# Kernel tuning notes

Measured on AMD Instinct MI355X. Metric: run time of the kernel, lower is better.

## Reference

```python
import jax, jax.numpy as jnp
import numpy as np

BANDWIDTH = 512.0


def _pairwise_lse(A, B, bandwidth):
    """logsumexp over all pairs of exp(-||a-b||^2 / bandwidth).

    Matches torch: vmap over rows b of B computing logsumexp over A,
    then logsumexp over those row results == single logsumexp over the
    full [Na, Nb] matrix of -sq_dist/bandwidth.
    """
    # squared distances via ||a||^2 + ||b||^2 - 2 a.b  (GEMM-dominated)
    a2 = jnp.sum(A * A, axis=-1)  # [Na]
    b2 = jnp.sum(B * B, axis=-1)  # [Nb]
    d2 = a2[:, None] + b2[None, :] - 2.0 * (A @ B.T)  # [Na, Nb]
    return jax.nn.logsumexp(-d2 / bandwidth)


def setup_inputs() -> dict:
    key = jax.random.key(0)
    kx, ky = jax.random.split(key)
    X = jax.random.normal(kx, (8192, 512), dtype=jnp.float32)
    Y = jax.random.normal(ky, (8192, 512), dtype=jnp.float32)
    return {"X": X, "Y": Y}


def reference(X, Y):
    n = X.shape[0]
    m = Y.shape[0]
    xx = (jnp.exp(_pairwise_lse(X, X, BANDWIDTH)) - n) / (n * (n - 1))
    xy = jnp.exp(_pairwise_lse(X, Y, BANDWIDTH)) / (n * m)
    yy = (jnp.exp(_pairwise_lse(Y, Y, BANDWIDTH)) - m) / (m * (m - 1))
    return xx - 2.0 * xy + yy
```

## Files before the change

### kernel.cpp

```cpp
#include <hip/hip_runtime.h>
#include <math.h>


#define D      512
#define BTM    128
#define BTN    256
#define BTNP   128
#define BK     16
#define KSTEPS (D / BK)

#define AHI 0
#define ALO 256
#define BHI 512
#define BLO 1024

typedef _Float16 half8 __attribute__((ext_vector_type(8)));
typedef __attribute__((ext_vector_type(8)))  short  short8;
typedef __attribute__((ext_vector_type(16))) float  f32x16;

union U4H8 { uint4 u; half8 h; };
union U4S8 { uint4 u; short8 s; };

__device__ __forceinline__ unsigned short bf16_rne(float x) {
    unsigned u = __float_as_uint(x);
    return (unsigned short)((u + 0x7fffu + ((u >> 16) & 1u)) >> 16);
}
__device__ __forceinline__ float bf16_f32(unsigned short b) {
    return __uint_as_float(((unsigned)b) << 16);
}
__device__ __forceinline__ void split8(const float v[8], uint4& hi, uint4& lo) {
    unsigned h[8], l[8];
    #pragma unroll
    for (int j = 0; j < 8; j++) {
        unsigned short bh = bf16_rne(v[j]);
        float r = v[j] - bf16_f32(bh);
        unsigned short bl = bf16_rne(r);
        h[j] = bh; l[j] = bl;
    }
    hi.x = h[0] | (h[1] << 16); hi.y = h[2] | (h[3] << 16);
    hi.z = h[4] | (h[5] << 16); hi.w = h[6] | (h[7] << 16);
    lo.x = l[0] | (l[1] << 16); lo.y = l[2] | (l[3] << 16);
    lo.z = l[4] | (l[5] << 16); lo.w = l[6] | (l[7] << 16);
}

__device__ __forceinline__ void lds16(const uint4* g, uint4* l) {
    __builtin_amdgcn_global_load_lds(
        (const __attribute__((address_space(1))) void*)g,
        (__attribute__((address_space(3))) void*)(unsigned int)(uintptr_t)(void*)l,
        16, 0, 0);
}

__global__ void init_kernel(double* accum, unsigned* minkey) {
    if (threadIdx.x < 3) accum[threadIdx.x] = 0.0;
    if (threadIdx.x < 4) minkey[threadIdx.x] = 0xFFFFFFFFu;
}

__global__ __launch_bounds__(256)
void convert_h_kernel(const float* __restrict__ X, const float* __restrict__ Y,
                      uint4* __restrict__ Xh, uint4* __restrict__ Yh, int npts) {
    const float* src = blockIdx.z ? Y : X;
    uint4*       dst = blockIdx.z ? Yh : Xh;
    const int ks = blockIdx.y;
    const int p  = blockIdx.x * 256 + threadIdx.x;
    if (p >= npts) return;
    const float* s = src + (size_t)p * D + ks * BK;
    float v[16];
    *(float4*)&v[0]  = *(const float4*)(s);
    *(float4*)&v[4]  = *(const float4*)(s + 4);
    *(float4*)&v[8]  = *(const float4*)(s + 8);
    *(float4*)&v[12] = *(const float4*)(s + 12);
    U4H8 a, b;
    #pragma unroll
    for (int j = 0; j < 8; j++) { a.h[j] = (_Float16)v[j]; b.h[j] = (_Float16)v[8 + j]; }
    size_t u = (size_t)ks * npts * 2 + (size_t)(p >> 5) * 64 + (p & 31);
    dst[u] = a.u; dst[u + 32] = b.u;
}

__global__ __launch_bounds__(256)
void row_norms_kernel(const float* __restrict__ X, const float* __restrict__ Y,
                      float* __restrict__ X2, float* __restrict__ Y2, int N, int M) {
    const int wave = threadIdx.x >> 6;
    const int lane = threadIdx.x & 63;
    const int row  = blockIdx.x * 4 + wave;
    const float* src; float* dst; int r;
    if (row < N)          { src = X; dst = X2; r = row; }
    else if (row < N + M) { src = Y; dst = Y2; r = row - N; }
    else return;
    const float* p = src + (size_t)r * D;
    float s = 0.f;
    #pragma unroll
    for (int c = 0; c < D; c += 64) {
        float v = p[c + lane];
        s = fmaf(v, v, s);
    }
    #pragma unroll
    for (int off = 32; off > 0; off >>= 1) s += __shfl_down(s, off);
    if (lane == 0) dst[r] = s;
}

__device__ inline unsigned float_key(float f) {
    unsigned u = __float_as_uint(f);
    return (u & 0x80000000u) ? ~u : (u | 0x80000000u);
}
__device__ inline float key_float(unsigned k) {
    return __uint_as_float((k & 0x80000000u) ? (k ^ 0x80000000u) : ~k);
}

__global__ __launch_bounds__(256)
void diag_min_bits_kernel(const float* __restrict__ X, const float* __restrict__ Y,
                          const float* __restrict__ X2, const float* __restrict__ Y2,
                          unsigned* __restrict__ minkey, int ngx) {
    int b = blockIdx.x;
    const float *src, *n2; int zidx;
    if (b < ngx) { src = X; n2 = X2; zidx = 0; }
    else         { src = Y; n2 = Y2; zidx = 2; b -= ngx; }

    const int tid  = threadIdx.x;
    const int wave = tid >> 6, lane = tid & 63;
    const int grp  = b * 4 + wave;
    const int fp   = lane & 31, fh = lane >> 5;
    const int pt   = grp * 32 + fp;
    const float* s = src + (size_t)pt * D + fh * 8;

    f32x16 acc;
    #pragma unroll
    for (int i = 0; i < 16; i++) acc[i] = 0.f;

    for (int ks = 0; ks < KSTEPS; ks++) {
        float v[8];
        *(float4*)&v[0] = *(const float4*)(s + ks * BK);
        *(float4*)&v[4] = *(const float4*)(s + ks * BK + 4);
        U4S8 hi, lo;
        split8(v, hi.u, lo.u);
        short8 ah = hi.s, al = lo.s;
        acc = __builtin_amdgcn_mfma_f32_32x32x16_bf16(ah, ah, acc, 0, 0, 0);
        acc = __builtin_amdgcn_mfma_f32_32x32x16_bf16(ah, al, acc, 0, 0, 0);
        acc = __builtin_amdgcn_mfma_f32_32x32x16_bf16(al, ah, acc, 0, 0, 0);
    }

    float dmin = 1e30f;
    if (fh == ((fp >> 2) & 1)) {
        int r = (fp & 3) + 4 * (fp >> 3);
        float av = acc[r];
        float rn = n2[pt];
        float cn = rn;
        float d2 = rn + cn - 2.0f * av;
        dmin = d2;
    }
    #pragma unroll
    for (int off = 32; off > 0; off >>= 1) dmin = fminf(dmin, __shfl_down(dmin, off));
    __shared__ float wm[4];
    __shared__ int   wz[4];
    if (lane == 0) { wm[wave] = dmin; wz[wave] = zidx; }
    __syncthreads();
    if (tid == 0)
        atomicMin(&minkey[wz[0]],
                  float_key(fminf(fminf(wm[0], wm[1]), fminf(wm[2], wm[3]))));
}

__global__ __launch_bounds__(256, 4)
void pair_exp_sum_kernel(const uint4* __restrict__ Xh, const uint4* __restrict__ Yh,
                         const float* __restrict__ X2, const float* __restrict__ Y2,
                         double* __restrict__ accum, float* __restrict__ bmin,
                         int N, int M) {
    const int z = blockIdx.z;
    const uint4 *Ah, *Bh; const float *An, *Bn; bool sym; int na, nb;
    if (z == 0)      { Ah = Xh; Bh = Xh; An = X2; Bn = X2; sym = true;  na = N; nb = N; }
    else if (z == 1) { Ah = Xh; Bh = Yh; An = X2; Bn = Y2; sym = false; na = N; nb = M; }
    else             { Ah = Yh; Bh = Yh; An = Y2; Bn = Y2; sym = true;  na = M; nb = M; }
    const int bi = blockIdx.x, bj = blockIdx.y;
    if (sym && bj < bi) return;

    __shared__ uint4  smem[2][1024];
    __shared__ float  smN[BTM + BTNP];
    __shared__ double wsum[4];
    __shared__ float  wmin[4];

    const int tid  = threadIdx.x;
    const int wave = tid >> 6, lane = tid & 63;
    const int wy = wave >> 1, wx = wave & 1;
    const int row0 = bi * BTM, col0 = bj * BTNP;

    if (tid < BTM) smN[tid] = An[row0 + tid];
    else           smN[tid] = Bn[col0 + tid - BTM];

    const size_t strideA = (size_t)na * 2;
    const size_t strideB = (size_t)nb * 2;
    const int sj = wave >> 1, skind = wave & 1;
    const uint4* gS = (skind ? Bh + (size_t)(col0 >> 5) * 64
                             : Ah + (size_t)(row0 >> 5) * 64) + lane;
    const size_t strideS = skind ? strideB : strideA;

    f32x16 acc[2][2];
    #pragma unroll
    for (int g = 0; g < 2; g++)
        #pragma unroll
        for (int c = 0; c < 2; c++)
            #pragma unroll
            for (int i = 0; i < 16; i++) acc[g][c][i] = 0.f;

    auto stage2 = [&](int buf, int ks) {
        const uint4* g = gS + (size_t)(ks + sj) * strideS;
        uint4* d = &smem[buf][sj * 512 + skind * 256 + lane];
        #pragma unroll
        for (int t = 0; t < 4; t++)
            lds16(g + t * 64, d + t * 64);
    };
    auto computeK = [&](const uint4* base) {
        const half8* p = (const half8*)base;
        half8 ah[2], bh[2];
        #pragma unroll
        for (int g = 0; g < 2; g++) ah[g] = p[(2 * wy + g) * 64 + lane];
        #pragma unroll
        for (int c = 0; c < 2; c++) bh[c] = p[256 + (2 * wx + c) * 64 + lane];
        #pragma unroll
        for (int g = 0; g < 2; g++)
            #pragma unroll
            for (int c = 0; c < 2; c++)
                acc[g][c] = __builtin_amdgcn_mfma_f32_32x32x16_f16(ah[g], bh[c], acc[g][c], 0, 0, 0);
    };

    stage2(0, 0);

    #pragma unroll
    for (int it = 1; it < KSTEPS / 2; it++) {
        stage2(it & 1, 2 * it);
        asm volatile("s_waitcnt vmcnt(4)" ::: "memory");
        __builtin_amdgcn_s_barrier();
        __builtin_amdgcn_sched_barrier(0);
        const int pb = (it - 1) & 1;
        computeK(&smem[pb][0]);
        computeK(&smem[pb][512]);
        asm volatile("s_waitcnt lgkmcnt(0)" ::: "memory");
        __builtin_amdgcn_s_barrier();
    }
    asm volatile("s_waitcnt vmcnt(0)" ::: "memory");
    __builtin_amdgcn_s_barrier();
    __builtin_amdgcn_sched_barrier(0);
    computeK(&smem[1][0]);
    computeK(&smem[1][512]);

    const float wgt = (sym && bj > bi) ? 2.f : 1.f;

    const int fp = lane & 31, fh = lane >> 5;
    double s = 0.0;
    float dmin = 1e30f;
    {
        const float* rowN = &smN[64 * wy];
        const float* colN = &smN[BTM + 64 * wx];
        const float kC = -0.0028177637517362567f;
        #pragma unroll
        for (int g = 0; g < 2; g++)
            #pragma unroll
            for (int c = 0; c < 2; c++) {
                float cn = colN[32 * c + fp];
                float rs = 0.f;
                #pragma unroll
                for (int r = 0; r < 16; r++) {
                    int r32 = (r & 3) + 8 * (r >> 2) + 4 * fh;
                    float d2 = rowN[32 * g + r32] + cn - 2.0f * acc[g][c][r];
                    dmin = fminf(dmin, d2);
                    rs += exp2f(d2 * kC);
                }
                s += (double)rs;
            }
        s *= (double)wgt;
    }

    #pragma unroll
    for (int off = 32; off > 0; off >>= 1) {
        s += __shfl_down(s, off);
        dmin = fminf(dmin, __shfl_down(dmin, off));
    }
    if (lane == 0) { wsum[wave] = s; wmin[wave] = dmin; }
    __syncthreads();
    if (tid == 0) {
        atomicAdd(&accum[z], wsum[0] + wsum[1] + wsum[2] + wsum[3]);
        if (z == 1)
            bmin[bi * gridDim.y + bj] = fminf(fminf(wmin[0], wmin[1]),
                                              fminf(wmin[2], wmin[3]));
    }
}

__global__ __launch_bounds__(256)
void xy_gmin_kernel(const float* __restrict__ bmin, float* __restrict__ gmin, int nblk) {
    float m = 1e30f;
    for (int i = threadIdx.x; i < nblk; i += 256) m = fminf(m, bmin[i]);
    #pragma unroll
    for (int off = 32; off > 0; off >>= 1) m = fminf(m, __shfl_down(m, off));
    __shared__ float wm[4];
    if ((threadIdx.x & 63) == 0) wm[threadIdx.x >> 6] = m;
    __syncthreads();
    if (threadIdx.x == 0) gmin[0] = fminf(fminf(wm[0], wm[1]), fminf(wm[2], wm[3]));
}

__global__ __launch_bounds__(1024)
void refine_min_kernel(const float* __restrict__ A, const float* __restrict__ B,
                       const float* __restrict__ An, const float* __restrict__ Bn,
                       const float* __restrict__ bmin, const float* __restrict__ gmin,
                       unsigned* __restrict__ minkey, int zidx, int nbj) {
    const int bi = blockIdx.x;
    const int bj = blockIdx.y;
    float bm = fminf(bmin[bi * nbj + 2 * bj], bmin[bi * nbj + 2 * bj + 1]);
    if (!(bm < gmin[0] + 0.5f)) return;
    const int row0 = bi * BTM, col0 = bj * BTN;

    __shared__ uint4 smem[1536];
    __shared__ float smN[BTM + BTN];
    __shared__ float wmin[16];

    const int tid  = threadIdx.x;
    const int wave = tid >> 6, lane = tid & 63;
    const int gy = wave & 3, cg0 = 2 * (wave >> 2);
    if (tid < BTM) smN[tid] = An[row0 + tid];
    if (tid < BTN) smN[BTM + tid] = Bn[col0 + tid];

    const int fp = lane & 31, fh = lane >> 5;
    const int au = (32 * gy + fp) * 2 + fh;
    int bu[2];
    #pragma unroll
    for (int c = 0; c < 2; c++) bu[c] = (32 * (cg0 + c) + fp) * 2 + fh;

    f32x16 acc[2];
    #pragma unroll
    for (int c = 0; c < 2; c++)
        #pragma unroll
        for (int i = 0; i < 16; i++) acc[c][i] = 0.f;

    for (int ks = 0; ks < KSTEPS; ks++) {
        __syncthreads();
        if (tid < 256) {
            const float* s = A + (size_t)(row0 + (tid >> 1)) * D + ks * BK + (tid & 1) * 8;
            float v[8];
            *(float4*)&v[0] = *(const float4*)s;
            *(float4*)&v[4] = *(const float4*)(s + 4);
            uint4 hi, lo; split8(v, hi, lo);
            smem[AHI + tid] = hi; smem[ALO + tid] = lo;
        } else if (tid < 768) {
            int u = tid - 256;
            const float* s = B + (size_t)(col0 + (u >> 1)) * D + ks * BK + (u & 1) * 8;
            float v[8];
            *(float4*)&v[0] = *(const float4*)s;
            *(float4*)&v[4] = *(const float4*)(s + 4);
            uint4 hi, lo; split8(v, hi, lo);
            smem[BHI + u] = hi; smem[BLO + u] = lo;
        }
        __syncthreads();
        {
            const short8* p = (const short8*)&smem[0];
            short8 ah = p[AHI + au], al = p[ALO + au];
            short8 bh[2], bl[2];
            #pragma unroll
            for (int c = 0; c < 2; c++) { bh[c] = p[BHI + bu[c]]; bl[c] = p[BLO + bu[c]]; }
            #pragma unroll
            for (int c = 0; c < 2; c++)
                acc[c] = __builtin_amdgcn_mfma_f32_32x32x16_bf16(ah, bh[c], acc[c], 0, 0, 0);
            #pragma unroll
            for (int c = 0; c < 2; c++)
                acc[c] = __builtin_amdgcn_mfma_f32_32x32x16_bf16(ah, bl[c], acc[c], 0, 0, 0);
            #pragma unroll
            for (int c = 0; c < 2; c++)
                acc[c] = __builtin_amdgcn_mfma_f32_32x32x16_bf16(al, bh[c], acc[c], 0, 0, 0);
        }
    }

    float dmin = 1e30f;
    const float* rowN = &smN[32 * gy];
    #pragma unroll
    for (int c = 0; c < 2; c++) {
        float cn = smN[BTM + 32 * (cg0 + c) + fp];
        #pragma unroll
        for (int r = 0; r < 16; r++) {
            int r32 = (r & 3) + 8 * (r >> 2) + 4 * fh;
            float d2 = rowN[r32] + cn - 2.0f * acc[c][r];
            dmin = fminf(dmin, d2);
        }
    }

    #pragma unroll
    for (int off = 32; off > 0; off >>= 1) dmin = fminf(dmin, __shfl_down(dmin, off));
    if (lane == 0) wmin[wave] = dmin;
    __syncthreads();
    if (tid == 0) {
        float m = wmin[0];
        #pragma unroll
        for (int w = 1; w < 16; w++) m = fminf(m, wmin[w]);
        atomicMin(&minkey[zidx], float_key(m));
    }
}

__global__ void finalize_kernel(const double* __restrict__ accum,
                                const unsigned* __restrict__ minkey,
                                float* __restrict__ out, int N, int M) {
    if (threadIdx.x == 0 && blockIdx.x == 0) {
        float Sp[3];
        #pragma unroll
        for (int z = 0; z < 3; z++) {
            float m = key_float(minkey[z]) * (-1.0f / 512.0f);
            double Sshift = accum[z] * exp(-(double)m);
            float r = (float)log(Sshift);
            float lse = r + m;
            Sp[z] = (float)exp((double)lse);
        }
        float nf  = (float)N, mf = (float)M;
        float nn1 = (float)((double)N * (double)(N - 1));
        float mm1 = (float)((double)M * (double)(M - 1));
        float nm  = (float)((double)N * (double)M);
        float xx = (Sp[0] - nf) / nn1;
        float xy =  Sp[1]       / nm;
        float yy = (Sp[2] - mf) / mm1;
        out[0] = xx - 2.0f * xy + yy;
    }
}

extern "C" void kernel_launch(void* const* d_in, const int* in_sizes, int n_in,
                              void* d_out, int out_size, void* d_ws, size_t ws_size,
                              hipStream_t stream) {
    const float* X = (const float*)d_in[0];
    const float* Y = (const float*)d_in[1];
    const int N = in_sizes[0] / D;
    const int M = in_sizes[1] / D;
    const int gx  = N / BTM;
    const int gyP = M / BTNP;
    const int gyR = M / BTN;

    double*   accum  = (double*)d_ws;
    unsigned* minkey = (unsigned*)((char*)d_ws + 32);
    float*    gmin   = (float*)((char*)d_ws + 48);
    float*    X2     = (float*)((char*)d_ws + 64);
    float*    Y2     = X2 + N;
    float*    bmin   = Y2 + M;
    size_t off = (64 + (size_t)(N + M) * 4 + (size_t)gx * gyP * 4 + 255) & ~(size_t)255;
    size_t asz = (size_t)N * D * 2;
    uint4* Xh = (uint4*)((char*)d_ws + off);
    uint4* Yh = (uint4*)((char*)d_ws + off + asz);

    init_kernel<<<1, 64, 0, stream>>>(accum, minkey);

    row_norms_kernel<<<(N + M + 3) / 4, 256, 0, stream>>>(X, Y, X2, Y2, N, M);
    convert_h_kernel<<<dim3((N + 255) / 256, KSTEPS, 2), 256, 0, stream>>>(X, Y, Xh, Yh, N);

    diag_min_bits_kernel<<<N / 128 + M / 128, 256, 0, stream>>>(X, Y, X2, Y2, minkey, N / 128);

    dim3 grid(gx, gyP, 3);
    pair_exp_sum_kernel<<<grid, 256, 0, stream>>>(Xh, Yh, X2, Y2, accum, bmin, N, M);

    xy_gmin_kernel<<<1, 256, 0, stream>>>(bmin, gmin, gx * gyP);
    refine_min_kernel<<<dim3(gx, gyR), 1024, 0, stream>>>(X, Y, X2, Y2, bmin, gmin,
                                                          minkey, 1, gyP);

    finalize_kernel<<<1, 64, 0, stream>>>(accum, minkey, (float*)d_out, N, M);
}
```

Baseline: 315.8 us.

## Enlarge pairwise GEMM tile to 256x256 with 8 waves and deeper K staging

Grows the pair_exp_sum block tile from 128x128 to 256x256 with 512 threads, so each wave computes a 128x64 subtile (4x2 MFMA 32x32 blocks). This raises arithmetic intensity and cuts global and LDS traffic per FLOP. The K loop now double-buffers 64-wide K chunks, staged in four 16-wide phases, and raises wave priority around the MFMA bursts. The refine kernel's block-min lookup is remapped to the coarser bmin grid. The cost is more registers, 128 KB of LDS, fewer blocks and coarser pruning granularity in refine_min.

```diff
diff --git a/kernel.cpp b/kernel.cpp
--- a/kernel.cpp
+++ b/kernel.cpp
@@ -5,7 +5,8 @@
 #define D      512
 #define BTM    128
 #define BTN    256
-#define BTNP   128
+#define BM2    256
+#define BN2    256
 #define BK     16
 #define KSTEPS (D / BK)
 
@@ -158,7 +159,7 @@
                   float_key(fminf(fminf(wm[0], wm[1]), fminf(wm[2], wm[3]))));
 }
 
-__global__ __launch_bounds__(256, 4)
+__global__ __launch_bounds__(512, 2)
 void pair_exp_sum_kernel(const uint4* __restrict__ Xh, const uint4* __restrict__ Yh,
                          const float* __restrict__ X2, const float* __restrict__ Y2,
                          double* __restrict__ accum, float* __restrict__ bmin,
@@ -171,74 +172,93 @@
     const int bi = blockIdx.x, bj = blockIdx.y;
     if (sym && bj < bi) return;
 
-    __shared__ uint4  smem[2][1024];
-    __shared__ float  smN[BTM + BTNP];
-    __shared__ double wsum[4];
-    __shared__ float  wmin[4];
+    __shared__ uint4  smem[2][4096];
+    __shared__ float  smN[BM2 + BN2];
+    __shared__ double wsum[8];
+    __shared__ float  wmin[8];
 
     const int tid  = threadIdx.x;
     const int wave = tid >> 6, lane = tid & 63;
-    const int wy = wave >> 1, wx = wave & 1;
-    const int row0 = bi * BTM, col0 = bj * BTNP;
-
-    if (tid < BTM) smN[tid] = An[row0 + tid];
-    else           smN[tid] = Bn[col0 + tid - BTM];
+    const int wy = wave >> 2, wx = wave & 3;
+    const int row0 = bi * BM2, col0 = bj * BN2;
+
+    float nval = (tid < BM2) ? An[row0 + tid] : Bn[col0 + tid - BM2];
+    asm volatile("s_waitcnt vmcnt(0)" ::: "memory");
+    smN[tid] = nval;
 
     const size_t strideA = (size_t)na * 2;
     const size_t strideB = (size_t)nb * 2;
-    const int sj = wave >> 1, skind = wave & 1;
-    const uint4* gS = (skind ? Bh + (size_t)(col0 >> 5) * 64
-                             : Ah + (size_t)(row0 >> 5) * 64) + lane;
-    const size_t strideS = skind ? strideB : strideA;
-
-    f32x16 acc[2][2];
-    #pragma unroll
-    for (int g = 0; g < 2; g++)
+    const uint4* gA = Ah + (size_t)(row0 >> 5) * 64 + wave * 64 + lane;
+    const uint4* gB = Bh + (size_t)(col0 >> 5) * 64 + wave * 64 + lane;
+
+    f32x16 acc[4][2];
+    #pragma unroll
+    for (int g = 0; g < 4; g++)
         #pragma unroll
         for (int c = 0; c < 2; c++)
             #pragma unroll
             for (int i = 0; i < 16; i++) acc[g][c][i] = 0.f;
 
-    auto stage2 = [&](int buf, int ks) {
-        const uint4* g = gS + (size_t)(ks + sj) * strideS;
-        uint4* d = &smem[buf][sj * 512 + skind * 256 + lane];
-        #pragma unroll
-        for (int t = 0; t < 4; t++)
-            lds16(g + t * 64, d + t * 64);
+    auto stage1 = [&](int buf, int p, int ktn) {
+        const int ksg = ktn * 4 + p;
+        lds16(gA + (size_t)ksg * strideA, &smem[buf][p * 1024 + wave * 64 + lane]);
+        lds16(gB + (size_t)ksg * strideB, &smem[buf][p * 1024 + 512 + wave * 64 + lane]);
     };
-    auto computeK = [&](const uint4* base) {
-        const half8* p = (const half8*)base;
-        half8 ah[2], bh[2];
-        #pragma unroll
-        for (int g = 0; g < 2; g++) ah[g] = p[(2 * wy + g) * 64 + lane];
-        #pragma unroll
-        for (int c = 0; c < 2; c++) bh[c] = p[256 + (2 * wx + c) * 64 + lane];
-        #pragma unroll
-        for (int g = 0; g < 2; g++)
-            #pragma unroll
-            for (int c = 0; c < 2; c++)
-                acc[g][c] = __builtin_amdgcn_mfma_f32_32x32x16_f16(ah[g], bh[c], acc[g][c], 0, 0, 0);
-    };
-
-    stage2(0, 0);
-
-    #pragma unroll
-    for (int it = 1; it < KSTEPS / 2; it++) {
-        stage2(it & 1, 2 * it);
-        asm volatile("s_waitcnt vmcnt(4)" ::: "memory");
-        __builtin_amdgcn_s_barrier();
-        __builtin_amdgcn_sched_barrier(0);
-        const int pb = (it - 1) & 1;
-        computeK(&smem[pb][0]);
-        computeK(&smem[pb][512]);
-        asm volatile("s_waitcnt lgkmcnt(0)" ::: "memory");
-        __builtin_amdgcn_s_barrier();
-    }
-    asm volatile("s_waitcnt vmcnt(0)" ::: "memory");
-    __builtin_amdgcn_s_barrier();
-    __builtin_amdgcn_sched_barrier(0);
-    computeK(&smem[1][0]);
-    computeK(&smem[1][512]);
+
+    #pragma unroll
+    for (int p = 0; p < 4; p++) stage1(0, p, 0);
+
+    for (int kt = 0; kt < 7; kt++) {
+        const int pb = kt & 1, nbuf = pb ^ 1;
+        #pragma unroll
+        for (int p = 0; p < 4; p++) {
+            stage1(nbuf, p, kt + 1);
+            asm volatile("s_waitcnt vmcnt(8)" ::: "memory");
+            __builtin_amdgcn_s_barrier();
+            __builtin_amdgcn_sched_barrier(0);
+            const half8* base = (const half8*)&smem[pb][p * 1024];
+            half8 ah[4], bh[2];
+            #pragma unroll
+            for (int g = 0; g < 4; g++) ah[g] = base[(4 * wy + g) * 64 + lane];
+            #pragma unroll
+            for (int c = 0; c < 2; c++) bh[c] = base[512 + (2 * wx + c) * 64 + lane];
+            asm volatile("s_waitcnt lgkmcnt(0)" ::: "memory");
+            __builtin_amdgcn_sched_barrier(0);
+            __builtin_amdgcn_s_setprio(1);
+            #pragma unroll
+            for (int g = 0; g < 4; g++)
+                #pragma unroll
+                for (int c = 0; c < 2; c++)
+                    acc[g][c] = __builtin_amdgcn_mfma_f32_32x32x16_f16(ah[g], bh[c], acc[g][c], 0, 0, 0);
+            __builtin_amdgcn_s_setprio(0);
+        }
+    }
+    {
+        #pragma unroll
+        for (int p = 0; p < 4; p++) {
+            if      (p == 0) asm volatile("s_waitcnt vmcnt(6)" ::: "memory");
+            else if (p == 1) asm volatile("s_waitcnt vmcnt(4)" ::: "memory");
+            else if (p == 2) asm volatile("s_waitcnt vmcnt(2)" ::: "memory");
+            else             asm volatile("s_waitcnt vmcnt(0)" ::: "memory");
+            __builtin_amdgcn_s_barrier();
+            __builtin_amdgcn_sched_barrier(0);
+            const half8* base = (const half8*)&smem[1][p * 1024];
+            half8 ah[4], bh[2];
+            #pragma unroll
+            for (int g = 0; g < 4; g++) ah[g] = base[(4 * wy + g) * 64 + lane];
+            #pragma unroll
+            for (int c = 0; c < 2; c++) bh[c] = base[512 + (2 * wx + c) * 64 + lane];
+            asm volatile("s_waitcnt lgkmcnt(0)" ::: "memory");
+            __builtin_amdgcn_sched_barrier(0);
+            __builtin_amdgcn_s_setprio(1);
+            #pragma unroll
+            for (int g = 0; g < 4; g++)
+                #pragma unroll
+                for (int c = 0; c < 2; c++)
+                    acc[g][c] = __builtin_amdgcn_mfma_f32_32x32x16_f16(ah[g], bh[c], acc[g][c], 0, 0, 0);
+            __builtin_amdgcn_s_setprio(0);
+        }
+    }
 
     const float wgt = (sym && bj > bi) ? 2.f : 1.f;
 
@@ -246,11 +266,11 @@
     double s = 0.0;
     float dmin = 1e30f;
     {
-        const float* rowN = &smN[64 * wy];
-        const float* colN = &smN[BTM + 64 * wx];
+        const float* rowN = &smN[128 * wy];
+        const float* colN = &smN[BM2 + 64 * wx];
         const float kC = -0.0028177637517362567f;
         #pragma unroll
-        for (int g = 0; g < 2; g++)
+        for (int g = 0; g < 4; g++)
             #pragma unroll
             for (int c = 0; c < 2; c++) {
                 float cn = colN[32 * c + fp];
@@ -275,10 +295,13 @@
     if (lane == 0) { wsum[wave] = s; wmin[wave] = dmin; }
     __syncthreads();
     if (tid == 0) {
-        atomicAdd(&accum[z], wsum[0] + wsum[1] + wsum[2] + wsum[3]);
+        double ts = wsum[0];
+        float  tm = wmin[0];
+        #pragma unroll
+        for (int w = 1; w < 8; w++) { ts += wsum[w]; tm = fminf(tm, wmin[w]); }
+        atomicAdd(&accum[z], ts);
         if (z == 1)
-            bmin[bi * gridDim.y + bj] = fminf(fminf(wmin[0], wmin[1]),
-                                              fminf(wmin[2], wmin[3]));
+            bmin[bi * gridDim.y + bj] = tm;
     }
 }
 
@@ -301,7 +324,7 @@
                        unsigned* __restrict__ minkey, int zidx, int nbj) {
     const int bi = blockIdx.x;
     const int bj = blockIdx.y;
-    float bm = fminf(bmin[bi * nbj + 2 * bj], bmin[bi * nbj + 2 * bj + 1]);
+    float bm = bmin[(bi >> 1) * nbj + bj];
     if (!(bm < gmin[0] + 0.5f)) return;
     const int row0 = bi * BTM, col0 = bj * BTN;
 
@@ -421,8 +444,9 @@
     const int N = in_sizes[0] / D;
     const int M = in_sizes[1] / D;
     const int gx  = N / BTM;
-    const int gyP = M / BTNP;
     const int gyR = M / BTN;
+    const int gx2 = N / BM2;
+    const int gy2 = M / BN2;
 
     double*   accum  = (double*)d_ws;
     unsigned* minkey = (unsigned*)((char*)d_ws + 32);
@@ -430,7 +454,7 @@
     float*    X2     = (float*)((char*)d_ws + 64);
     float*    Y2     = X2 + N;
     float*    bmin   = Y2 + M;
-    size_t off = (64 + (size_t)(N + M) * 4 + (size_t)gx * gyP * 4 + 255) & ~(size_t)255;
+    size_t off = (64 + (size_t)(N + M) * 4 + (size_t)gx2 * gy2 * 4 + 255) & ~(size_t)255;
     size_t asz = (size_t)N * D * 2;
     uint4* Xh = (uint4*)((char*)d_ws + off);
     uint4* Yh = (uint4*)((char*)d_ws + off + asz);
@@ -442,12 +466,12 @@
 
     diag_min_bits_kernel<<<N / 128 + M / 128, 256, 0, stream>>>(X, Y, X2, Y2, minkey, N / 128);
 
-    dim3 grid(gx, gyP, 3);
-    pair_exp_sum_kernel<<<grid, 256, 0, stream>>>(Xh, Yh, X2, Y2, accum, bmin, N, M);
-
-    xy_gmin_kernel<<<1, 256, 0, stream>>>(bmin, gmin, gx * gyP);
+    dim3 grid(gx2, gy2, 3);
+    pair_exp_sum_kernel<<<grid, 512, 0, stream>>>(Xh, Yh, X2, Y2, accum, bmin, N, M);
+
+    xy_gmin_kernel<<<1, 256, 0, stream>>>(bmin, gmin, gx2 * gy2);
     refine_min_kernel<<<dim3(gx, gyR), 1024, 0, stream>>>(X, Y, X2, Y2, bmin, gmin,
-                                                          minkey, 1, gyP);
+                                                          minkey, 1, gy2);
 
     finalize_kernel<<<1, 64, 0, stream>>>(accum, minkey, (float*)d_out, N, M);
 }
```

New measurement: 351.6 us. +11.3%, slower.
